# Kernel tuning notes

Hardware: AMD Instinct MI355X
Metric: run time of the kernel (lower is better)

The kernel has to match this reference:

```python
import jax, jax.numpy as jnp
import numpy as np

P, M, DG, F, H, DH = 2000, 150, 2000, 256, 4, 64
N1, N2 = P + M, P + DG          # adj1 nodes (patient+med), adj2 nodes (patient+diag)
E1, E2, EGP, EGM = 137600, 256000, 64000, 4800
GNN_LAYERS = 2
SA_HID = 128


def setup_inputs() -> dict:
    key = jax.random.key(0)
    ks = jax.random.split(key, 32)
    ri = lambda k, n, hi: jax.random.randint(k, (n,), 0, hi, dtype=jnp.int32)
    rn = lambda k, shape, scale: (jax.random.normal(k, shape, dtype=jnp.float32) * scale)
    inp = {
        'adj1_rows': ri(ks[0], E1, N1), 'adj1_cols': ri(ks[1], E1, N1),
        'adj1_vals': jax.random.uniform(ks[2], (E1,), dtype=jnp.float32),
        'adj2_rows': ri(ks[3], E2, N2), 'adj2_cols': ri(ks[4], E2, N2),
        'adj2_vals': jax.random.uniform(ks[5], (E2,), dtype=jnp.float32),
        'g0_src': ri(ks[6], EGP, P), 'g0_dst': ri(ks[7], EGP, P),
        'g1_src': ri(ks[8], EGP, P), 'g1_dst': ri(ks[9], EGP, P),
        'g2_src': ri(ks[10], EGM, M), 'g2_dst': ri(ks[11], EGM, M),
        'g3_src': ri(ks[12], EGM, M), 'g3_dst': ri(ks[13], EGM, M),
        'keepRate': 1,
        # learned parameters (xavier-ish scales)
        'pEmbed': rn(ks[14], (P, F), 0.05),
        'mEmbed': rn(ks[15], (M, F), 0.05),
        'dEmbed': rn(ks[16], (DG, F), 0.05),
        'gat_W': rn(ks[17], (4, F, H * DH), (2.0 / (F + H * DH)) ** 0.5),
        'gat_al': rn(ks[18], (4, H, DH), 0.1),
        'gat_ar': rn(ks[19], (4, H, DH), 0.1),
        'gat_b': jnp.zeros((4, H * DH), dtype=jnp.float32),
        'sa_W1': rn(ks[20], (H * DH, SA_HID), (2.0 / (H * DH + SA_HID)) ** 0.5),
        'sa_b1': jnp.zeros((SA_HID,), dtype=jnp.float32),
        'sa_W2': rn(ks[21], (SA_HID, 1), 0.1),
        'out_W': rn(ks[22], (2 * F, M), (2.0 / (2 * F + M)) ** 0.5),
        'out_b': jnp.zeros((M,), dtype=jnp.float32),
    }
    return inp


def _spmm(rows, cols, vals, x, n):
    # sparse adj @ x via gather + segment_sum
    return jax.ops.segment_sum(vals[:, None] * x[cols], rows, num_segments=n)


def _seg_softmax(e, seg, n):
    m = jax.ops.segment_max(e, seg, num_segments=n)          # [n, H]
    ex = jnp.exp(e - m[seg])
    s = jax.ops.segment_sum(ex, seg, num_segments=n)
    return ex / (s[seg] + 1e-9)


def _gat(h, W, al, ar, b, src, dst, n):
    # DGL GATConv, feat/attn dropout = 0, negative_slope = 0.2, activation = elu
    feat = (h @ W).reshape(n, H, DH)                          # [n, H, DH]
    el = (feat * al[None]).sum(-1)                            # [n, H]
    er = (feat * ar[None]).sum(-1)
    e = jax.nn.leaky_relu(el[src] + er[dst], negative_slope=0.2)  # [E, H]
    alpha = _seg_softmax(e, dst, n)                           # softmax over in-edges per dst
    out = jax.ops.segment_sum(alpha[:, :, None] * feat[src], dst, num_segments=n)
    out = out + b.reshape(1, H, DH)
    return jax.nn.elu(out).reshape(n, H * DH)


def _sem_att(z, W1, b1, W2):
    # z: [N, K, F]; shared projection; beta over K meta-paths
    w = (jnp.tanh(z @ W1 + b1) @ W2).mean(0)                  # [K, 1]
    beta = jax.nn.softmax(w, axis=0)                          # [K, 1]
    return (beta[None] * z).sum(1)                            # [N, F]


def reference(adj1_rows, adj1_cols, adj1_vals, adj2_rows, adj2_cols, adj2_vals,
              g0_src, g0_dst, g1_src, g1_dst, g2_src, g2_dst, g3_src, g3_dst,
              keepRate, pEmbed, mEmbed, dEmbed, gat_W, gat_al, gat_ar, gat_b,
              sa_W1, sa_b1, sa_W2, out_W, out_b):
    embeds1 = jnp.concatenate([pEmbed, mEmbed], axis=0)       # [N1, F]
    embeds2 = jnp.concatenate([pEmbed, dEmbed], axis=0)       # [N2, F]
    lat1, lat2 = embeds1, embeds2
    acc1 = jnp.zeros_like(embeds1)
    acc2 = jnp.zeros_like(embeds2)
    for _ in range(GNN_LAYERS):
        lat1 = jax.nn.leaky_relu(_spmm(adj1_rows, adj1_cols, adj1_vals, lat1, N1), negative_slope=0.5)
        lat2 = jax.nn.leaky_relu(_spmm(adj2_rows, adj2_cols, adj2_vals, lat2, N2), negative_slope=0.5)
        acc1 = acc1 + lat1
        acc2 = acc2 + lat2
    p1, m_gcn = acc1[:P], acc1[P:]
    p2, d_gcn = acc2[:P], acc2[P:]

    e0 = _gat(p1, gat_W[0], gat_al[0], gat_ar[0], gat_b[0], g0_src, g0_dst, P)
    e1 = _gat(p2, gat_W[1], gat_al[1], gat_ar[1], gat_b[1], g1_src, g1_dst, P)
    e2 = _gat(m_gcn, gat_W[2], gat_al[2], gat_ar[2], gat_b[2], g2_src, g2_dst, M)
    e3 = _gat(m_gcn, gat_W[3], gat_al[3], gat_ar[3], gat_b[3], g3_src, g3_dst, M)

    patient = _sem_att(jnp.stack([e0, e1], axis=1), sa_W1, sa_b1, sa_W2)  # [P, F]
    med = _sem_att(jnp.stack([e2, e3], axis=1), sa_W1, sa_b1, sa_W2)      # [M, F]

    # broadcasted pairwise concat -> ReLU -> Linear -> sum over pairing axis
    pm = jnp.concatenate([
        jnp.broadcast_to(patient[:, None, :], (P, M, F)),
        jnp.broadcast_to(med[None, :, :], (P, M, F)),
    ], axis=-1).reshape(P * M, 2 * F)
    simi = (jax.nn.relu(pm) @ out_W + out_b).reshape(P, M, M)
    simi_pm = simi.sum(axis=1)                                # [P, M]
    return (simi_pm, d_gcn, med, m_gcn, patient)
```

## Files before the change

### kernel.cpp

```cpp
#include <hip/hip_runtime.h>
#include <hip/hip_fp16.h>
#include <cmath>
#include <cstdint>

constexpr int P  = 2000, M = 150, DG = 2000, F = 256, H = 4, DH = 64;
constexpr int N1 = P + M;
constexpr int N2 = P + DG;
constexpr int E1 = 137600, E2 = 256000, EGP = 64000, EGM = 4800;
constexpr int SA_HID = 128;

constexpr int HO1 = E1, HO2 = E1 + E2, HO3 = HO2 + EGP, HO4 = HO3 + EGP,
              HO5 = HO4 + EGM, HOE = HO5 + EGM;

constexpr int CAP_A = 160;
constexpr int CAP_G = 96;
constexpr int OVF_CAP = 4096;

constexpr int CPAD = 16;

__device__ __forceinline__ float4 h4_to_f4(const __half* p) {
  union { ushort4 u4; __half2 h2[2]; } u;
  u.u4 = *(const ushort4*)p;
  float2 lo = __half22float2(u.h2[0]);
  float2 hi = __half22float2(u.h2[1]);
  return make_float4(lo.x, lo.y, hi.x, hi.y);
}
__device__ __forceinline__ void f4_to_h4(__half* p, float4 v) {
  union { ushort4 u4; __half2 h2[2]; } u;
  u.h2[0] = __float22half2_rn(make_float2(v.x, v.y));
  u.h2[1] = __float22half2_rn(make_float2(v.z, v.w));
  *(ushort4*)p = u.u4;
}

constexpr int CAST_CH = (P * F + M * F + DG * F) / 8;

__global__ __launch_bounds__(256) void k_build(
    const int* __restrict__ a1r, const int* __restrict__ a1c, const float* __restrict__ a1v,
    const int* __restrict__ a2r, const int* __restrict__ a2c, const float* __restrict__ a2v,
    const int* __restrict__ d0, const int* __restrict__ s0,
    const int* __restrict__ d1, const int* __restrict__ s1,
    const int* __restrict__ d2, const int* __restrict__ s2,
    const int* __restrict__ d3, const int* __restrict__ s3,
    int* cur1, uint2* ell1, int* cur2, uint2* ell2,
    int* cu0, unsigned* eg0, int* cu1, unsigned* eg1,
    int* cu2, unsigned* eg2, int* cu3, unsigned* eg3,
    int* __restrict__ ovf_n, int4* __restrict__ ovf,
    const float* __restrict__ pEf, const float* __restrict__ mEf,
    const float* __restrict__ dEf,
    __half* __restrict__ pEh, __half* __restrict__ mEh, __half* __restrict__ dEh) {
  int tid = blockIdx.x * 256 + threadIdx.x;
  int T = gridDim.x * 256;
  int seg[4], row[4]; unsigned p0[4], p1[4];
#pragma unroll
  for (int u = 0; u < 4; ++u) {
    int i = tid + u * T;
    seg[u] = -1;
    if (i < HOE) {
      if (i < HO1)      { seg[u] = 0; row[u] = a1r[i]; p0[u] = (unsigned)a1c[i]; p1[u] = __float_as_uint(a1v[i]); }
      else if (i < HO2) { int j = i - HO1; seg[u] = 1; row[u] = a2r[j]; p0[u] = (unsigned)a2c[j]; p1[u] = __float_as_uint(a2v[j]); }
      else if (i < HO3) { int j = i - HO2; seg[u] = 2; row[u] = d0[j]; p0[u] = (unsigned)s0[j]; }
      else if (i < HO4) { int j = i - HO3; seg[u] = 3; row[u] = d1[j]; p0[u] = (unsigned)s1[j]; }
      else if (i < HO5) { int j = i - HO4; seg[u] = 4; row[u] = d2[j]; p0[u] = (unsigned)s2[j]; }
      else              { int j = i - HO5; seg[u] = 5; row[u] = d3[j]; p0[u] = (unsigned)s3[j]; }
    }
  }
#pragma unroll
  for (int u = 0; u < 4; ++u) {
    int r = row[u];
    switch (seg[u]) {
      case 0: { int slot = atomicAdd(&cur1[(size_t)r * CPAD], 1);
        if (slot < CAP_A) ell1[(size_t)r * CAP_A + slot] = make_uint2(p0[u], p1[u]);
        else { int o = atomicAdd(&ovf_n[0], 1); if (o < OVF_CAP) ovf[0 * OVF_CAP + o] = make_int4(r, (int)p0[u], (int)p1[u], 0); } } break;
      case 1: { int slot = atomicAdd(&cur2[(size_t)r * CPAD], 1);
        if (slot < CAP_A) ell2[(size_t)r * CAP_A + slot] = make_uint2(p0[u], p1[u]);
        else { int o = atomicAdd(&ovf_n[1], 1); if (o < OVF_CAP) ovf[1 * OVF_CAP + o] = make_int4(r, (int)p0[u], (int)p1[u], 0); } } break;
      case 2: { int slot = atomicAdd(&cu0[(size_t)r * CPAD], 1);
        if (slot < CAP_G) eg0[(size_t)r * CAP_G + slot] = p0[u];
        else { int o = atomicAdd(&ovf_n[2], 1); if (o < OVF_CAP) ovf[2 * OVF_CAP + o] = make_int4(r, (int)p0[u], 0, 0); } } break;
      case 3: { int slot = atomicAdd(&cu1[(size_t)r * CPAD], 1);
        if (slot < CAP_G) eg1[(size_t)r * CAP_G + slot] = p0[u];
        else { int o = atomicAdd(&ovf_n[3], 1); if (o < OVF_CAP) ovf[3 * OVF_CAP + o] = make_int4(r, (int)p0[u], 0, 0); } } break;
      case 4: { int slot = atomicAdd(&cu2[(size_t)r * CPAD], 1);
        if (slot < CAP_G) eg2[(size_t)r * CAP_G + slot] = p0[u];
        else { int o = atomicAdd(&ovf_n[4], 1); if (o < OVF_CAP) ovf[4 * OVF_CAP + o] = make_int4(r, (int)p0[u], 0, 0); } } break;
      case 5: { int slot = atomicAdd(&cu3[(size_t)r * CPAD], 1);
        if (slot < CAP_G) eg3[(size_t)r * CAP_G + slot] = p0[u];
        else { int o = atomicAdd(&ovf_n[5], 1); if (o < OVF_CAP) ovf[5 * OVF_CAP + o] = make_int4(r, (int)p0[u], 0, 0); } } break;
      default: break;
    }
  }
  for (int c = tid; c < CAST_CH; c += T) {
    int j = c * 8;
    const float* src; __half* dst;
    if (j < P * F)              { src = pEf + j;               dst = pEh + j; }
    else if (j < P * F + M * F) { src = mEf + (j - P * F);     dst = mEh + (j - P * F); }
    else                        { src = dEf + (j - P*F - M*F); dst = dEh + (j - P*F - M*F); }
    float4 a = *(const float4*)src, b = *(const float4*)(src + 4);
    f4_to_h4(dst, a);
    f4_to_h4(dst + 4, b);
  }
}

template<int LAYER>
__global__ __launch_bounds__(256) void k_spmm(
    const int* __restrict__ cur1, const uint2* __restrict__ ell1,
    const int* __restrict__ cur2, const uint2* __restrict__ ell2,
    const int* __restrict__ ovf_n, const int4* __restrict__ ovf,
    const __half* __restrict__ pEh, const __half* __restrict__ mEh,
    const __half* __restrict__ dEh,
    float* __restrict__ lat1f, float* __restrict__ lat2f,
    __half* __restrict__ lat1h, __half* __restrict__ lat2h,
    float* __restrict__ acc1, float* __restrict__ acc2,
    float* __restrict__ out_mgcn, float* __restrict__ out_dgcn) {
  int grp = (blockIdx.x * 256 + threadIdx.x) >> 7;
  int lane = threadIdx.x & 63;
  int wh   = (threadIdx.x >> 6) & 1;
  int gl   = threadIdx.x >> 7;
  bool g2 = grp >= N1;
  int row = g2 ? grp - N1 : grp;
  const uint2* pe = (g2 ? ell2 : ell1) + (size_t)row * CAP_A;
  const __half* latinh = g2 ? lat2h : lat1h;
  const __half* tailEh = g2 ? dEh : mEh;
  int deg = (g2 ? cur2 : cur1)[(size_t)row * CPAD];
  int dn = deg < CAP_A ? deg : CAP_A;
  int fo = lane << 2;
  float4 s = {0.f, 0.f, 0.f, 0.f};
  auto fetch = [&](int c) -> float4 {
    const __half* b;
    if (LAYER == 1) b = (c < P) ? (pEh + (size_t)c * F) : (tailEh + (size_t)(c - P) * F);
    else            b = latinh + (size_t)c * F;
    return h4_to_f4(b + fo);
  };
  int i = wh;
  for (; i + 15 <= dn; i += 16) {
    uint2 m[8]; float4 a[8];
#pragma unroll
    for (int u = 0; u < 8; ++u) m[u] = pe[i + 2 * u];
#pragma unroll
    for (int u = 0; u < 8; ++u) a[u] = fetch((int)m[u].x);
#pragma unroll
    for (int u = 0; u < 8; ++u) {
      float v = __uint_as_float(m[u].y);
      s.x += v * a[u].x; s.y += v * a[u].y; s.z += v * a[u].z; s.w += v * a[u].w;
    }
  }
  for (; i < dn; i += 2) {
    uint2 m = pe[i];
    float v = __uint_as_float(m.y);
    float4 a = fetch((int)m.x);
    s.x += v * a.x; s.y += v * a.y; s.z += v * a.z; s.w += v * a.w;
  }
  __shared__ float part[2][F];
  if (wh == 1) *(float4*)&part[gl][fo] = s;
  __syncthreads();
  if (wh == 1) return;
  {
    float4 p = *(const float4*)&part[gl][fo];
    s.x += p.x; s.y += p.y; s.z += p.z; s.w += p.w;
  }
  {
    int gi = g2 ? 1 : 0;
    int on = ovf_n[gi];
    if (on > 0) {
      const int4* ol = ovf + gi * OVF_CAP;
      for (int k = 0; k < on; ++k) {
        int4 e = ol[k];
        if (e.x == row) {
          float v = __int_as_float(e.z);
          float4 a = fetch(e.y);
          s.x += v * a.x; s.y += v * a.y; s.z += v * a.z; s.w += v * a.w;
        }
      }
    }
  }
  float4 l;
  l.x = s.x > 0.f ? s.x : 0.5f * s.x;
  l.y = s.y > 0.f ? s.y : 0.5f * s.y;
  l.z = s.z > 0.f ? s.z : 0.5f * s.z;
  l.w = s.w > 0.f ? s.w : 0.5f * s.w;
  if (LAYER == 1) {
    *(float4*)((g2 ? lat2f : lat1f) + (size_t)row * F + fo) = l;
    f4_to_h4((g2 ? lat2h : lat1h) + (size_t)row * F + fo, l);
  } else {
    const float* latf = g2 ? lat2f : lat1f;
    float4 b = *(const float4*)(latf + (size_t)row * F + fo);
    float4 a = {b.x + l.x, b.y + l.y, b.z + l.z, b.w + l.w};
    *(float4*)((g2 ? acc2 : acc1) + (size_t)row * F + fo) = a;
    if (row >= P)
      *(float4*)((g2 ? out_dgcn : out_mgcn) + (size_t)(row - P) * F + fo) = a;
  }
}

constexpr int FR  = 8;
constexpr int NB0 = (P + FR - 1) / FR;
constexpr int NB2 = (M + FR - 1) / FR;
constexpr int FEAT_BLOCKS = 2 * NB0 + 2 * NB2;

__global__ __launch_bounds__(256) void k_gat_feat_all(
    const float* __restrict__ acc1, const float* __restrict__ acc2,
    const float* __restrict__ gat_W, const float* __restrict__ gat_al,
    const float* __restrict__ gat_ar,
    __half* __restrict__ f0, __half* __restrict__ f1,
    __half* __restrict__ f2, __half* __restrict__ f3,
    float* __restrict__ el, float* __restrict__ er) {
  int b = blockIdx.x;
  int g, rb, n; const float* h; __half* fout;
  if (b < NB0)            { g = 0; rb = b;              n = P; h = acc1; fout = f0; }
  else if (b < 2 * NB0)   { g = 1; rb = b - NB0;        n = P; h = acc2; fout = f1; }
  else if (b < 2*NB0+NB2) { g = 2; rb = b - 2 * NB0;    n = M; h = acc1 + (size_t)P * F; fout = f2; }
  else                    { g = 3; rb = b - 2*NB0 - NB2; n = M; h = acc1 + (size_t)P * F; fout = f3; }
  int elo = (g == 0) ? 0 : (g == 1) ? P * H : (g == 2) ? 2 * P * H : (2 * P + M) * H;
  const float* W = gat_W + (size_t)g * F * F;
  __shared__ float hs[FR][F];
  int t = threadIdx.x;
  int r0 = rb * FR;
  for (int q = t; q < FR * 64; q += 256) {
    int r = q >> 6, ln = q & 63;
    int row = r0 + r;
    float4 v = {0.f, 0.f, 0.f, 0.f};
    if (row < n) v = *(const float4*)(h + (size_t)row * F + (ln << 2));
    *(float4*)&hs[r][ln << 2] = v;
  }
  __syncthreads();
  float acc[FR];
#pragma unroll
  for (int r = 0; r < FR; ++r) acc[r] = 0.f;
  for (int k = 0; k < F; k += 4) {
    float w0 = W[(size_t)k * F + t],       w1 = W[(size_t)(k + 1) * F + t],
          w2 = W[(size_t)(k + 2) * F + t], w3 = W[(size_t)(k + 3) * F + t];
#pragma unroll
    for (int r = 0; r < FR; ++r) {
      float4 h4 = *(const float4*)&hs[r][k];
      acc[r] += h4.x * w0 + h4.y * w1 + h4.z * w2 + h4.w * w3;
    }
  }
  int head = t >> 6, d = t & 63;
  float av = gat_al[g * H * DH + head * DH + d];
  float rv = gat_ar[g * H * DH + head * DH + d];
#pragma unroll
  for (int r = 0; r < FR; ++r) {
    int row = r0 + r;
    if (row < n) {
      fout[(size_t)row * F + t] = __float2half_rn(acc[r]);
      float cl = acc[r] * av, cr = acc[r] * rv;
      for (int o = 32; o > 0; o >>= 1) {
        cl += __shfl_down(cl, o, 64);
        cr += __shfl_down(cr, o, 64);
      }
      if (d == 0) { el[elo + row * H + head] = cl; er[elo + row * H + head] = cr; }
    }
  }
}

__global__ __launch_bounds__(256) void k_gat_agg_all(
    const int* __restrict__ cu0, const unsigned* __restrict__ eg0,
    const int* __restrict__ cu1, const unsigned* __restrict__ eg1,
    const int* __restrict__ cu2, const unsigned* __restrict__ eg2,
    const int* __restrict__ cu3, const unsigned* __restrict__ eg3,
    const int* __restrict__ ovf_n, const int4* __restrict__ ovf,
    const float* __restrict__ el, const float* __restrict__ er,
    const __half* __restrict__ f0, const __half* __restrict__ f1,
    const __half* __restrict__ f2, const __half* __restrict__ f3,
    const float* __restrict__ gat_b,
    float* __restrict__ e0, float* __restrict__ e1,
    float* __restrict__ e2, float* __restrict__ e3) {
  int grp = (blockIdx.x * 256 + threadIdx.x) >> 7;
  int lane = threadIdx.x & 63;
  int wh   = (threadIdx.x >> 6) & 1;
  int gl   = threadIdx.x >> 7;
  int g, row; const int* cu; const unsigned* eg; const __half* feat; float* out; int elo;
  if (grp < P)            { g = 0; row = grp;             cu = cu0; eg = eg0; feat = f0; out = e0; elo = 0; }
  else if (grp < 2 * P)   { g = 1; row = grp - P;         cu = cu1; eg = eg1; feat = f1; out = e1; elo = P * H; }
  else if (grp < 2*P + M) { g = 2; row = grp - 2 * P;     cu = cu2; eg = eg2; feat = f2; out = e2; elo = 2 * P * H; }
  else                    { g = 3; row = grp - 2 * P - M; cu = cu3; eg = eg3; feat = f3; out = e3; elo = (2 * P + M) * H; }
  int head = lane >> 4;
  int fo = lane << 2;
  const float* elb = el + elo;
  float erv = er[elo + row * H + head];
  int deg = cu[(size_t)row * CPAD];
  int dn = deg < CAP_G ? deg : CAP_G;
  const unsigned* ps = eg + (size_t)row * CAP_G;
  int on = ovf_n[2 + g];
  const int4* ol = ovf + (2 + g) * OVF_CAP;
  float mx = -3.4e38f;
  int i = wh;
  for (; i + 7 <= dn; i += 8) {
    int s0 = (int)ps[i], s1 = (int)ps[i + 2], s2 = (int)ps[i + 4], s3 = (int)ps[i + 6];
    float a = elb[s0 * H + head] + erv, b = elb[s1 * H + head] + erv,
          c = elb[s2 * H + head] + erv, d = elb[s3 * H + head] + erv;
    a = a > 0.f ? a : 0.2f * a; b = b > 0.f ? b : 0.2f * b;
    c = c > 0.f ? c : 0.2f * c; d = d > 0.f ? d : 0.2f * d;
    mx = fmaxf(mx, fmaxf(fmaxf(a, b), fmaxf(c, d)));
  }
  for (; i < dn; i += 2) {
    float a = elb[(int)ps[i] * H + head] + erv;
    a = a > 0.f ? a : 0.2f * a;
    mx = fmaxf(mx, a);
  }
  if (wh == 0 && on > 0) {
    for (int k = 0; k < on; ++k) {
      int4 e = ol[k];
      if (e.x == row) {
        float a = elb[e.y * H + head] + erv;
        a = a > 0.f ? a : 0.2f * a;
        mx = fmaxf(mx, a);
      }
    }
  }
  __shared__ float mxs[2][2][64];
  mxs[gl][wh][lane] = mx;
  __syncthreads();
  mx = fmaxf(mxs[gl][0][lane], mxs[gl][1][lane]);
  float ssum = 0.f;
  float4 acc = {0.f, 0.f, 0.f, 0.f};
  i = wh;
  for (; i + 7 <= dn; i += 8) {
    int s0 = (int)ps[i], s1 = (int)ps[i + 2], s2 = (int)ps[i + 4], s3 = (int)ps[i + 6];
    float a = elb[s0 * H + head] + erv; a = a > 0.f ? a : 0.2f * a;
    float b = elb[s1 * H + head] + erv; b = b > 0.f ? b : 0.2f * b;
    float c = elb[s2 * H + head] + erv; c = c > 0.f ? c : 0.2f * c;
    float d = elb[s3 * H + head] + erv; d = d > 0.f ? d : 0.2f * d;
    float x0 = expf(a - mx), x1 = expf(b - mx), x2 = expf(c - mx), x3 = expf(d - mx);
    float4 q0 = h4_to_f4(feat + (size_t)s0 * F + fo);
    float4 q1 = h4_to_f4(feat + (size_t)s1 * F + fo);
    float4 q2 = h4_to_f4(feat + (size_t)s2 * F + fo);
    float4 q3 = h4_to_f4(feat + (size_t)s3 * F + fo);
    ssum += (x0 + x1) + (x2 + x3);
    acc.x += x0 * q0.x + x1 * q1.x + x2 * q2.x + x3 * q3.x;
    acc.y += x0 * q0.y + x1 * q1.y + x2 * q2.y + x3 * q3.y;
    acc.z += x0 * q0.z + x1 * q1.z + x2 * q2.z + x3 * q3.z;
    acc.w += x0 * q0.w + x1 * q1.w + x2 * q2.w + x3 * q3.w;
  }
  for (; i + 3 <= dn; i += 4) {
    int s0 = (int)ps[i], s1 = (int)ps[i + 2];
    float a = elb[s0 * H + head] + erv; a = a > 0.f ? a : 0.2f * a;
    float b = elb[s1 * H + head] + erv; b = b > 0.f ? b : 0.2f * b;
    float x0 = expf(a - mx), x1 = expf(b - mx);
    float4 q0 = h4_to_f4(feat + (size_t)s0 * F + fo);
    float4 q1 = h4_to_f4(feat + (size_t)s1 * F + fo);
    ssum += x0 + x1;
    acc.x += x0 * q0.x + x1 * q1.x;
    acc.y += x0 * q0.y + x1 * q1.y;
    acc.z += x0 * q0.z + x1 * q1.z;
    acc.w += x0 * q0.w + x1 * q1.w;
  }
  for (; i < dn; i += 2) {
    int s0 = (int)ps[i];
    float a = elb[s0 * H + head] + erv; a = a > 0.f ? a : 0.2f * a;
    float x0 = expf(a - mx);
    float4 q0 = h4_to_f4(feat + (size_t)s0 * F + fo);
    ssum += x0;
    acc.x += x0 * q0.x; acc.y += x0 * q0.y; acc.z += x0 * q0.z; acc.w += x0 * q0.w;
  }
  __shared__ float4 pacc[2][64];
  __shared__ float  pss[2][64];
  if (wh == 1) { pacc[gl][lane] = acc; pss[gl][lane] = ssum; }
  __syncthreads();
  if (wh == 1) return;
  {
    float4 pa = pacc[gl][lane];
    acc.x += pa.x; acc.y += pa.y; acc.z += pa.z; acc.w += pa.w;
    ssum += pss[gl][lane];
  }
  if (on > 0) {
    for (int k = 0; k < on; ++k) {
      int4 e = ol[k];
      if (e.x == row) {
        float a = elb[e.y * H + head] + erv; a = a > 0.f ? a : 0.2f * a;
        float x0 = expf(a - mx);
        float4 q0 = h4_to_f4(feat + (size_t)e.y * F + fo);
        ssum += x0;
        acc.x += x0 * q0.x; acc.y += x0 * q0.y; acc.z += x0 * q0.z; acc.w += x0 * q0.w;
      }
    }
  }
  float inv = 1.f / (ssum + 1e-9f);
  const float* bb = gat_b + g * F + fo;
  float4 v = {acc.x * inv + bb[0], acc.y * inv + bb[1],
              acc.z * inv + bb[2], acc.w * inv + bb[3]};
  v.x = v.x > 0.f ? v.x : expm1f(v.x);
  v.y = v.y > 0.f ? v.y : expm1f(v.y);
  v.z = v.z > 0.f ? v.z : expm1f(v.z);
  v.w = v.w > 0.f ? v.w : expm1f(v.w);
  *(float4*)(out + (size_t)row * F + fo) = v;
}

constexpr int SR  = 4;
constexpr int SB0 = (P + SR - 1) / SR;
constexpr int SB2 = (M + SR - 1) / SR;
constexpr int SEM_BLOCKS = 2 * SB0 + 2 * SB2;

__global__ __launch_bounds__(128) void k_sem_w_all(
    const float* __restrict__ e0, const float* __restrict__ e1,
    const float* __restrict__ e2, const float* __restrict__ e3,
    const float* __restrict__ W1, const float* __restrict__ b1,
    const float* __restrict__ W2, float* __restrict__ w) {
  int b = blockIdx.x;
  int zid, rb, n; const float* z;
  if (b < SB0)            { zid = 0; rb = b;             n = P; z = e0; }
  else if (b < 2 * SB0)   { zid = 1; rb = b - SB0;       n = P; z = e1; }
  else if (b < 2*SB0+SB2) { zid = 2; rb = b - 2 * SB0;   n = M; z = e2; }
  else                    { zid = 3; rb = b - 2*SB0-SB2; n = M; z = e3; }
  __shared__ float zs[SR][F];
  int t = threadIdx.x;
  int r0 = rb * SR;
  for (int q = t; q < SR * 64; q += 128) {
    int r = q >> 6, ln = q & 63;
    int row = r0 + r;
    float4 v = {0.f, 0.f, 0.f, 0.f};
    if (row < n) v = *(const float4*)(z + (size_t)row * F + (ln << 2));
    *(float4*)&zs[r][ln << 2] = v;
  }
  __syncthreads();
  float hid[SR];
#pragma unroll
  for (int r = 0; r < SR; ++r) hid[r] = b1[t];
  for (int k = 0; k < F; k += 4) {
    float w0 = W1[(size_t)k * SA_HID + t],       w1 = W1[(size_t)(k + 1) * SA_HID + t],
          w2 = W1[(size_t)(k + 2) * SA_HID + t], w3 = W1[(size_t)(k + 3) * SA_HID + t];
#pragma unroll
    for (int r = 0; r < SR; ++r) {
      float4 z4 = *(const float4*)&zs[r][k];
      hid[r] += z4.x * w0 + z4.y * w1 + z4.z * w2 + z4.w * w3;
    }
  }
  float w2v = W2[t];
  float local = 0.f;
  for (int r = 0; r < SR; ++r) {
    int row = r0 + r;
    if (row < n) local += tanhf(hid[r]) * w2v;
  }
  for (int o = 32; o > 0; o >>= 1) local += __shfl_down(local, o, 64);
  __shared__ float pp[2];
  if ((t & 63) == 0) pp[t >> 6] = local;
  __syncthreads();
  if (t == 0) atomicAdd(&w[zid], pp[0] + pp[1]);
}

constexpr int FIN_R = 4;
__global__ __launch_bounds__(256) void k_final_all(
    const float* __restrict__ e0, const float* __restrict__ e1,
    const float* __restrict__ e2, const float* __restrict__ e3,
    const float* __restrict__ w, const float* __restrict__ outW,
    const float* __restrict__ outb,
    float* __restrict__ out_med, float* __restrict__ out_pat,
    float* __restrict__ simi) {
  int t = threadIdx.x;
  float mm0 = w[2] * (1.f / M), mm1 = w[3] * (1.f / M);
  float mmx = fmaxf(mm0, mm1);
  float bm0 = expf(mm0 - mmx), bm1 = expf(mm1 - mmx);
  float msc = 1.f / (bm0 + bm1);
  bm0 *= msc; bm1 *= msc;
  float pm0 = w[0] * (1.f / P), pm1 = w[1] * (1.f / P);
  float pmx = fmaxf(pm0, pm1);
  float bp0 = expf(pm0 - pmx), bp1 = expf(pm1 - pmx);
  float psc = 1.f / (bp0 + bp1);
  bp0 *= psc; bp1 *= psc;
  int r0 = blockIdx.x * FIN_R;
  int pr = t >> 6, pln = t & 63;
  size_t poff = (size_t)(r0 + pr) * F + (pln << 2);
  float4 pu0 = *(const float4*)(e0 + poff);
  float4 pu1 = *(const float4*)(e1 + poff);
  constexpr int MED4 = M * F / 4;
  float4 rs = {0.f, 0.f, 0.f, 0.f};
  bool wr_med = (blockIdx.x == 0);
  for (int j = t; j < MED4; j += 512) {
    float4 u0 = ((const float4*)e2)[j], u1 = ((const float4*)e3)[j];
    float4 v0, v1;
    bool second = (j + 256) < MED4;
    if (second) { v0 = ((const float4*)e2)[j + 256]; v1 = ((const float4*)e3)[j + 256]; }
    float4 r = {bm0 * u0.x + bm1 * u1.x, bm0 * u0.y + bm1 * u1.y,
                bm0 * u0.z + bm1 * u1.z, bm0 * u0.w + bm1 * u1.w};
    if (wr_med) ((float4*)out_med)[j] = r;
    rs.x += r.x > 0.f ? r.x : 0.f;
    rs.y += r.y > 0.f ? r.y : 0.f;
    rs.z += r.z > 0.f ? r.z : 0.f;
    rs.w += r.w > 0.f ? r.w : 0.f;
    if (second) {
      float4 r2 = {bm0 * v0.x + bm1 * v1.x, bm0 * v0.y + bm1 * v1.y,
                   bm0 * v0.z + bm1 * v1.z, bm0 * v0.w + bm1 * v1.w};
      if (wr_med) ((float4*)out_med)[j + 256] = r2;
      rs.x += r2.x > 0.f ? r2.x : 0.f;
      rs.y += r2.y > 0.f ? r2.y : 0.f;
      rs.z += r2.z > 0.f ? r2.z : 0.f;
      rs.w += r2.w > 0.f ? r2.w : 0.f;
    }
  }
  __shared__ float psh[FIN_R][F];
  {
    float4 v = {bp0 * pu0.x + bp1 * pu1.x, bp0 * pu0.y + bp1 * pu1.y,
                bp0 * pu0.z + bp1 * pu1.z, bp0 * pu0.w + bp1 * pu1.w};
    *(float4*)(out_pat + poff) = v;
    v.x = v.x > 0.f ? v.x : 0.f; v.y = v.y > 0.f ? v.y : 0.f;
    v.z = v.z > 0.f ? v.z : 0.f; v.w = v.w > 0.f ? v.w : 0.f;
    *(float4*)&psh[pr][pln << 2] = v;
  }
  __shared__ float4 sv4[4][64];
  sv4[t >> 6][t & 63] = rs;
  __syncthreads();
  __shared__ float sv[F];
  if (t < 64) {
    float4 a = sv4[0][t], b = sv4[1][t], c = sv4[2][t], d = sv4[3][t];
    sv[t * 4 + 0] = a.x + b.x + c.x + d.x;
    sv[t * 4 + 1] = a.y + b.y + c.y + d.y;
    sv[t * 4 + 2] = a.z + b.z + c.z + d.z;
    sv[t * 4 + 3] = a.w + b.w + c.w + d.w;
  }
  __syncthreads();
  if (t < M) {
    float acc[FIN_R];
#pragma unroll
    for (int r = 0; r < FIN_R; ++r) acc[r] = 0.f;
    float cv = (float)M * outb[t];
    for (int f = 0; f < F; f += 4) {
      float w0 = outW[(size_t)f * M + t],       w1 = outW[(size_t)(f + 1) * M + t],
            w2 = outW[(size_t)(f + 2) * M + t], w3 = outW[(size_t)(f + 3) * M + t];
      float b0 = outW[(size_t)(F + f) * M + t],     b1 = outW[(size_t)(F + f + 1) * M + t],
            b2 = outW[(size_t)(F + f + 2) * M + t], b3 = outW[(size_t)(F + f + 3) * M + t];
      cv += sv[f] * b0 + sv[f + 1] * b1 + sv[f + 2] * b2 + sv[f + 3] * b3;
#pragma unroll
      for (int r = 0; r < FIN_R; ++r) {
        float4 p4 = *(const float4*)&psh[r][f];
        acc[r] += p4.x * w0 + p4.y * w1 + p4.z * w2 + p4.w * w3;
      }
    }
#pragma unroll
    for (int r = 0; r < FIN_R; ++r)
      simi[(size_t)(r0 + r) * M + t] = (float)M * acc[r] + cv;
  }
}

extern "C" void kernel_launch(void* const* d_in, const int* in_sizes, int n_in,
                              void* d_out, int out_size, void* d_ws, size_t ws_size,
                              hipStream_t stream) {
  const int*   adj1_rows = (const int*)d_in[0];
  const int*   adj1_cols = (const int*)d_in[1];
  const float* adj1_vals = (const float*)d_in[2];
  const int*   adj2_rows = (const int*)d_in[3];
  const int*   adj2_cols = (const int*)d_in[4];
  const float* adj2_vals = (const float*)d_in[5];
  const int*   g0_src = (const int*)d_in[6];
  const int*   g0_dst = (const int*)d_in[7];
  const int*   g1_src = (const int*)d_in[8];
  const int*   g1_dst = (const int*)d_in[9];
  const int*   g2_src = (const int*)d_in[10];
  const int*   g2_dst = (const int*)d_in[11];
  const int*   g3_src = (const int*)d_in[12];
  const int*   g3_dst = (const int*)d_in[13];
  const float* pE     = (const float*)d_in[15];
  const float* mE     = (const float*)d_in[16];
  const float* dE     = (const float*)d_in[17];
  const float* gat_W  = (const float*)d_in[18];
  const float* gat_al = (const float*)d_in[19];
  const float* gat_ar = (const float*)d_in[20];
  const float* gat_b  = (const float*)d_in[21];
  const float* sa_W1  = (const float*)d_in[22];
  const float* sa_b1  = (const float*)d_in[23];
  const float* sa_W2  = (const float*)d_in[24];
  const float* out_W  = (const float*)d_in[25];
  const float* out_b  = (const float*)d_in[26];

  int* ip = (int*)d_ws;
  int* cur1 = ip; ip += (size_t)N1 * CPAD;
  int* cur2 = ip; ip += (size_t)N2 * CPAD;
  int* cu0  = ip; ip += (size_t)P * CPAD;
  int* cu1  = ip; ip += (size_t)P * CPAD;
  int* cu2  = ip; ip += (size_t)M * CPAD;
  int* cu3  = ip; ip += (size_t)M * CPAD;
  int* ovf_n = ip; ip += 6;
  float* wbuf = (float*)ip; ip += 4;
  size_t memset_bytes = (size_t)((char*)ip - (char*)d_ws);

  uintptr_t up = ((uintptr_t)ip + 15) & ~(uintptr_t)15;
  int4* ovf = (int4*)up;
  uint2* ell1 = (uint2*)(ovf + 6 * OVF_CAP);
  uint2* ell2 = ell1 + (size_t)N1 * CAP_A;
  unsigned* eg0 = (unsigned*)(ell2 + (size_t)N2 * CAP_A);
  unsigned* eg1 = eg0 + (size_t)P * CAP_G;
  unsigned* eg2 = eg1 + (size_t)P * CAP_G;
  unsigned* eg3 = eg2 + (size_t)M * CAP_G;
  __half* hp = (__half*)(eg3 + (size_t)M * CAP_G);
  __half* pEh   = hp; hp += (size_t)P * F;
  __half* mEh   = hp; hp += (size_t)M * F;
  __half* dEh   = hp; hp += (size_t)DG * F;
  __half* lat1h = hp; hp += (size_t)N1 * F;
  __half* lat2h = hp; hp += (size_t)N2 * F;
  __half* f0h   = hp; hp += (size_t)P * F;
  __half* f1h   = hp; hp += (size_t)P * F;
  __half* f2h   = hp; hp += (size_t)M * F;
  __half* f3h   = hp; hp += (size_t)M * F;
  float* fp = (float*)hp;
  float* lat1f = fp; fp += (size_t)N1 * F;
  float* lat2f = fp; fp += (size_t)N2 * F;
  float* acc1  = fp; fp += (size_t)N1 * F;
  float* acc2  = fp; fp += (size_t)N2 * F;
  float* el    = fp; fp += (size_t)(2 * P + 2 * M) * H;
  float* er    = fp; fp += (size_t)(2 * P + 2 * M) * H;
  float* e0b   = fp; fp += (size_t)P * F;
  float* e1b   = fp; fp += (size_t)P * F;
  float* e2b   = fp; fp += (size_t)M * F;
  float* e3b   = fp; fp += (size_t)M * F;

  float* out_simi = (float*)d_out;
  float* out_dgcn = out_simi + (size_t)P * M;
  float* out_med  = out_dgcn + (size_t)DG * F;
  float* out_mgcn = out_med  + (size_t)M * F;
  float* out_pat  = out_mgcn + (size_t)M * F;

  hipMemsetAsync(d_ws, 0, memset_bytes, stream);

  int eb = ((HOE + 3) / 4 + 255) / 256;
  k_build<<<eb, 256, 0, stream>>>(adj1_rows, adj1_cols, adj1_vals,
                                  adj2_rows, adj2_cols, adj2_vals,
                                  g0_dst, g0_src, g1_dst, g1_src,
                                  g2_dst, g2_src, g3_dst, g3_src,
                                  cur1, ell1, cur2, ell2,
                                  cu0, eg0, cu1, eg1, cu2, eg2, cu3, eg3,
                                  ovf_n, ovf,
                                  pE, mE, dE, pEh, mEh, dEh);

  int sb = (N1 + N2) / 2;
  k_spmm<1><<<sb, 256, 0, stream>>>(cur1, ell1, cur2, ell2, ovf_n, ovf,
                                    pEh, mEh, dEh, lat1f, lat2f, lat1h, lat2h,
                                    acc1, acc2, out_mgcn, out_dgcn);
  k_spmm<2><<<sb, 256, 0, stream>>>(cur1, ell1, cur2, ell2, ovf_n, ovf,
                                    pEh, mEh, dEh, lat1f, lat2f, lat1h, lat2h,
                                    acc1, acc2, out_mgcn, out_dgcn);

  k_gat_feat_all<<<FEAT_BLOCKS, 256, 0, stream>>>(acc1, acc2, gat_W, gat_al, gat_ar,
                                                  f0h, f1h, f2h, f3h, el, er);
  int ab = (2 * P + 2 * M) / 2;
  k_gat_agg_all<<<ab, 256, 0, stream>>>(cu0, eg0, cu1, eg1, cu2, eg2, cu3, eg3,
                                        ovf_n, ovf, el, er, f0h, f1h, f2h, f3h, gat_b,
                                        e0b, e1b, e2b, e3b);

  k_sem_w_all<<<SEM_BLOCKS, 128, 0, stream>>>(e0b, e1b, e2b, e3b, sa_W1, sa_b1, sa_W2, wbuf);

  k_final_all<<<P / FIN_R, 256, 0, stream>>>(e0b, e1b, e2b, e3b, wbuf, out_W, out_b,
                                             out_med, out_pat, out_simi);
}
```

Before: 304.6 us.

## Use 16-byte gathers in SpMM and single-pass online softmax in GAT aggregation

The SpMM kernel now has each half-wavefront handle a different neighbor, loading 8 halves (16 bytes) per lane. The two halves are combined with a cross-lane shuffle, which halves the number of load instructions per edge. The GAT aggregation kernel replaces its separate max pass with an online softmax that rescales the running sum and accumulator, then merges the two wavefront partials with max-aware scaling. This removes a second traversal over the edge list and the el gathers, at the cost of extra exp calls and multiplies per step.

New measurement: 340.1 us. 11.6% more time.

```diff
diff --git a/kernel.cpp b/kernel.cpp
--- a/kernel.cpp
+++ b/kernel.cpp
@@ -30,6 +30,16 @@
   u.h2[0] = __float22half2_rn(make_float2(v.x, v.y));
   u.h2[1] = __float22half2_rn(make_float2(v.z, v.w));
   *(ushort4*)p = u.u4;
+}
+__device__ __forceinline__ void h8_to_f8(const __half* p, float4& lo, float4& hi) {
+  union { uint4 u; __half2 h2[4]; } uu;
+  uu.u = *(const uint4*)p;
+  float2 a0 = __half22float2(uu.h2[0]);
+  float2 a1 = __half22float2(uu.h2[1]);
+  float2 a2 = __half22float2(uu.h2[2]);
+  float2 a3 = __half22float2(uu.h2[3]);
+  lo = make_float4(a0.x, a0.y, a1.x, a1.y);
+  hi = make_float4(a2.x, a2.y, a3.x, a3.y);
 }
 
 constexpr int CAST_CH = (P * F + M * F + DG * F) / 8;
@@ -116,6 +126,9 @@
   int lane = threadIdx.x & 63;
   int wh   = (threadIdx.x >> 6) & 1;
   int gl   = threadIdx.x >> 7;
+  int half = lane >> 5;
+  int hl   = lane & 31;
+  int fo8  = hl << 3;
   bool g2 = grp >= N1;
   int row = g2 ? grp - N1 : grp;
   const uint2* pe = (g2 ? ell2 : ell1) + (size_t)row * CAP_A;
@@ -123,40 +136,65 @@
   const __half* tailEh = g2 ? dEh : mEh;
   int deg = (g2 ? cur2 : cur1)[(size_t)row * CPAD];
   int dn = deg < CAP_A ? deg : CAP_A;
-  int fo = lane << 2;
-  float4 s = {0.f, 0.f, 0.f, 0.f};
-  auto fetch = [&](int c) -> float4 {
-    const __half* b;
-    if (LAYER == 1) b = (c < P) ? (pEh + (size_t)c * F) : (tailEh + (size_t)(c - P) * F);
-    else            b = latinh + (size_t)c * F;
-    return h4_to_f4(b + fo);
+  float4 sA = {0.f, 0.f, 0.f, 0.f}, sB = {0.f, 0.f, 0.f, 0.f};
+  auto base = [&](int c) -> const __half* {
+    if (LAYER == 1) return (c < P) ? (pEh + (size_t)c * F) : (tailEh + (size_t)(c - P) * F);
+    return latinh + (size_t)c * F;
+  };
+  auto fetch8 = [&](int c, float4& lo, float4& hi) {
+    h8_to_f8(base(c) + fo8, lo, hi);
   };
   int i = wh;
   for (; i + 15 <= dn; i += 16) {
-    uint2 m[8]; float4 a[8];
+    uint2 m[8];
 #pragma unroll
     for (int u = 0; u < 8; ++u) m[u] = pe[i + 2 * u];
-#pragma unroll
-    for (int u = 0; u < 8; ++u) a[u] = fetch((int)m[u].x);
-#pragma unroll
-    for (int u = 0; u < 8; ++u) {
-      float v = __uint_as_float(m[u].y);
-      s.x += v * a[u].x; s.y += v * a[u].y; s.z += v * a[u].z; s.w += v * a[u].w;
-    }
-  }
-  for (; i < dn; i += 2) {
-    uint2 m = pe[i];
-    float v = __uint_as_float(m.y);
-    float4 a = fetch((int)m.x);
-    s.x += v * a.x; s.y += v * a.y; s.z += v * a.z; s.w += v * a.w;
-  }
+    float4 lo[4], hi[4];
+#pragma unroll
+    for (int u = 0; u < 4; ++u) {
+      uint2 me = half ? m[2 * u + 1] : m[2 * u];
+      fetch8((int)me.x, lo[u], hi[u]);
+    }
+#pragma unroll
+    for (int u = 0; u < 4; ++u) {
+      uint2 me = half ? m[2 * u + 1] : m[2 * u];
+      float v = __uint_as_float(me.y);
+      sA.x += v * lo[u].x; sA.y += v * lo[u].y; sA.z += v * lo[u].z; sA.w += v * lo[u].w;
+      sB.x += v * hi[u].x; sB.y += v * hi[u].y; sB.z += v * hi[u].z; sB.w += v * hi[u].w;
+    }
+  }
+  for (; i + 3 <= dn; i += 4) {
+    uint2 m0 = pe[i], m1 = pe[i + 2];
+    uint2 me = half ? m1 : m0;
+    float4 lo, hi; fetch8((int)me.x, lo, hi);
+    float v = __uint_as_float(me.y);
+    sA.x += v * lo.x; sA.y += v * lo.y; sA.z += v * lo.z; sA.w += v * lo.w;
+    sB.x += v * hi.x; sB.y += v * hi.y; sB.z += v * hi.z; sB.w += v * hi.w;
+  }
+  if (i < dn) {
+    uint2 m0 = pe[i];
+    uint2 me = half ? make_uint2(0u, 0u) : m0;
+    float4 lo, hi; fetch8((int)me.x, lo, hi);
+    float v = __uint_as_float(me.y);
+    sA.x += v * lo.x; sA.y += v * lo.y; sA.z += v * lo.z; sA.w += v * lo.w;
+    sB.x += v * hi.x; sB.y += v * hi.y; sB.z += v * hi.z; sB.w += v * hi.w;
+  }
+  sA.x += __shfl_down(sA.x, 32, 64); sA.y += __shfl_down(sA.y, 32, 64);
+  sA.z += __shfl_down(sA.z, 32, 64); sA.w += __shfl_down(sA.w, 32, 64);
+  sB.x += __shfl_down(sB.x, 32, 64); sB.y += __shfl_down(sB.y, 32, 64);
+  sB.z += __shfl_down(sB.z, 32, 64); sB.w += __shfl_down(sB.w, 32, 64);
   __shared__ float part[2][F];
-  if (wh == 1) *(float4*)&part[gl][fo] = s;
+  if (wh == 1 && half == 0) {
+    *(float4*)&part[gl][fo8]     = sA;
+    *(float4*)&part[gl][fo8 + 4] = sB;
+  }
   __syncthreads();
   if (wh == 1) return;
-  {
-    float4 p = *(const float4*)&part[gl][fo];
-    s.x += p.x; s.y += p.y; s.z += p.z; s.w += p.w;
+  if (half == 0) {
+    float4 pa = *(const float4*)&part[gl][fo8];
+    float4 pb = *(const float4*)&part[gl][fo8 + 4];
+    sA.x += pa.x; sA.y += pa.y; sA.z += pa.z; sA.w += pa.w;
+    sB.x += pb.x; sB.y += pb.y; sB.z += pb.z; sB.w += pb.w;
   }
   {
     int gi = g2 ? 1 : 0;
@@ -167,27 +205,46 @@
         int4 e = ol[k];
         if (e.x == row) {
           float v = __int_as_float(e.z);
-          float4 a = fetch(e.y);
-          s.x += v * a.x; s.y += v * a.y; s.z += v * a.z; s.w += v * a.w;
+          float4 lo, hi; fetch8(e.y, lo, hi);
+          sA.x += v * lo.x; sA.y += v * lo.y; sA.z += v * lo.z; sA.w += v * lo.w;
+          sB.x += v * hi.x; sB.y += v * hi.y; sB.z += v * hi.z; sB.w += v * hi.w;
         }
       }
     }
   }
-  float4 l;
-  l.x = s.x > 0.f ? s.x : 0.5f * s.x;
-  l.y = s.y > 0.f ? s.y : 0.5f * s.y;
-  l.z = s.z > 0.f ? s.z : 0.5f * s.z;
-  l.w = s.w > 0.f ? s.w : 0.5f * s.w;
+  if (half != 0) return;
+  float4 lA, lB;
+  lA.x = sA.x > 0.f ? sA.x : 0.5f * sA.x;
+  lA.y = sA.y > 0.f ? sA.y : 0.5f * sA.y;
+  lA.z = sA.z > 0.f ? sA.z : 0.5f * sA.z;
+  lA.w = sA.w > 0.f ? sA.w : 0.5f * sA.w;
+  lB.x = sB.x > 0.f ? sB.x : 0.5f * sB.x;
+  lB.y = sB.y > 0.f ? sB.y : 0.5f * sB.y;
+  lB.z = sB.z > 0.f ? sB.z : 0.5f * sB.z;
+  lB.w = sB.w > 0.f ? sB.w : 0.5f * sB.w;
+  size_t off = (size_t)row * F + fo8;
   if (LAYER == 1) {
-    *(float4*)((g2 ? lat2f : lat1f) + (size_t)row * F + fo) = l;
-    f4_to_h4((g2 ? lat2h : lat1h) + (size_t)row * F + fo, l);
+    float* lf = (g2 ? lat2f : lat1f);
+    *(float4*)(lf + off) = lA;
+    *(float4*)(lf + off + 4) = lB;
+    __half* lh = (g2 ? lat2h : lat1h);
+    f4_to_h4(lh + off, lA);
+    f4_to_h4(lh + off + 4, lB);
   } else {
     const float* latf = g2 ? lat2f : lat1f;
-    float4 b = *(const float4*)(latf + (size_t)row * F + fo);
-    float4 a = {b.x + l.x, b.y + l.y, b.z + l.z, b.w + l.w};
-    *(float4*)((g2 ? acc2 : acc1) + (size_t)row * F + fo) = a;
-    if (row >= P)
-      *(float4*)((g2 ? out_dgcn : out_mgcn) + (size_t)(row - P) * F + fo) = a;
+    float4 b0 = *(const float4*)(latf + off);
+    float4 b1 = *(const float4*)(latf + off + 4);
+    float4 a0 = {b0.x + lA.x, b0.y + lA.y, b0.z + lA.z, b0.w + lA.w};
+    float4 a1 = {b1.x + lB.x, b1.y + lB.y, b1.z + lB.z, b1.w + lB.w};
+    float* ac = (g2 ? acc2 : acc1);
+    *(float4*)(ac + off) = a0;
+    *(float4*)(ac + off + 4) = a1;
+    if (row >= P) {
+      float* og = (g2 ? out_dgcn : out_mgcn);
+      size_t ooff = (size_t)(row - P) * F + fo8;
+      *(float4*)(og + ooff) = a0;
+      *(float4*)(og + ooff + 4) = a1;
+    }
   }
 }
 
@@ -282,95 +339,92 @@
   const unsigned* ps = eg + (size_t)row * CAP_G;
   int on = ovf_n[2 + g];
   const int4* ol = ovf + (2 + g) * OVF_CAP;
-  float mx = -3.4e38f;
+  float m = -3.4e38f, ssum = 0.f;
+  float4 acc = {0.f, 0.f, 0.f, 0.f};
   int i = wh;
-  for (; i + 7 <= dn; i += 8) {
-    int s0 = (int)ps[i], s1 = (int)ps[i + 2], s2 = (int)ps[i + 4], s3 = (int)ps[i + 6];
-    float a = elb[s0 * H + head] + erv, b = elb[s1 * H + head] + erv,
-          c = elb[s2 * H + head] + erv, d = elb[s3 * H + head] + erv;
-    a = a > 0.f ? a : 0.2f * a; b = b > 0.f ? b : 0.2f * b;
-    c = c > 0.f ? c : 0.2f * c; d = d > 0.f ? d : 0.2f * d;
-    mx = fmaxf(mx, fmaxf(fmaxf(a, b), fmaxf(c, d)));
-  }
-  for (; i < dn; i += 2) {
-    float a = elb[(int)ps[i] * H + head] + erv;
-    a = a > 0.f ? a : 0.2f * a;
-    mx = fmaxf(mx, a);
-  }
-  if (wh == 0 && on > 0) {
-    for (int k = 0; k < on; ++k) {
-      int4 e = ol[k];
-      if (e.x == row) {
-        float a = elb[e.y * H + head] + erv;
-        a = a > 0.f ? a : 0.2f * a;
-        mx = fmaxf(mx, a);
-      }
-    }
-  }
-  __shared__ float mxs[2][2][64];
-  mxs[gl][wh][lane] = mx;
-  __syncthreads();
-  mx = fmaxf(mxs[gl][0][lane], mxs[gl][1][lane]);
-  float ssum = 0.f;
-  float4 acc = {0.f, 0.f, 0.f, 0.f};
-  i = wh;
   for (; i + 7 <= dn; i += 8) {
     int s0 = (int)ps[i], s1 = (int)ps[i + 2], s2 = (int)ps[i + 4], s3 = (int)ps[i + 6];
     float a = elb[s0 * H + head] + erv; a = a > 0.f ? a : 0.2f * a;
     float b = elb[s1 * H + head] + erv; b = b > 0.f ? b : 0.2f * b;
     float c = elb[s2 * H + head] + erv; c = c > 0.f ? c : 0.2f * c;
     float d = elb[s3 * H + head] + erv; d = d > 0.f ? d : 0.2f * d;
-    float x0 = expf(a - mx), x1 = expf(b - mx), x2 = expf(c - mx), x3 = expf(d - mx);
+    float nm = fmaxf(m, fmaxf(fmaxf(a, b), fmaxf(c, d)));
+    float sc = expf(m - nm);
+    float x0 = expf(a - nm), x1 = expf(b - nm), x2 = expf(c - nm), x3 = expf(d - nm);
     float4 q0 = h4_to_f4(feat + (size_t)s0 * F + fo);
     float4 q1 = h4_to_f4(feat + (size_t)s1 * F + fo);
     float4 q2 = h4_to_f4(feat + (size_t)s2 * F + fo);
     float4 q3 = h4_to_f4(feat + (size_t)s3 * F + fo);
-    ssum += (x0 + x1) + (x2 + x3);
-    acc.x += x0 * q0.x + x1 * q1.x + x2 * q2.x + x3 * q3.x;
-    acc.y += x0 * q0.y + x1 * q1.y + x2 * q2.y + x3 * q3.y;
-    acc.z += x0 * q0.z + x1 * q1.z + x2 * q2.z + x3 * q3.z;
-    acc.w += x0 * q0.w + x1 * q1.w + x2 * q2.w + x3 * q3.w;
+    ssum = ssum * sc + (x0 + x1) + (x2 + x3);
+    acc.x = acc.x * sc + x0 * q0.x + x1 * q1.x + x2 * q2.x + x3 * q3.x;
+    acc.y = acc.y * sc + x0 * q0.y + x1 * q1.y + x2 * q2.y + x3 * q3.y;
+    acc.z = acc.z * sc + x0 * q0.z + x1 * q1.z + x2 * q2.z + x3 * q3.z;
+    acc.w = acc.w * sc + x0 * q0.w + x1 * q1.w + x2 * q2.w + x3 * q3.w;
+    m = nm;
   }
   for (; i + 3 <= dn; i += 4) {
     int s0 = (int)ps[i], s1 = (int)ps[i + 2];
     float a = elb[s0 * H + head] + erv; a = a > 0.f ? a : 0.2f * a;
     float b = elb[s1 * H + head] + erv; b = b > 0.f ? b : 0.2f * b;
-    float x0 = expf(a - mx), x1 = expf(b - mx);
+    float nm = fmaxf(m, fmaxf(a, b));
+    float sc = expf(m - nm);
+    float x0 = expf(a - nm), x1 = expf(b - nm);
     float4 q0 = h4_to_f4(feat + (size_t)s0 * F + fo);
     float4 q1 = h4_to_f4(feat + (size_t)s1 * F + fo);
-    ssum += x0 + x1;
-    acc.x += x0 * q0.x + x1 * q1.x;
-    acc.y += x0 * q0.y + x1 * q1.y;
-    acc.z += x0 * q0.z + x1 * q1.z;
-    acc.w += x0 * q0.w + x1 * q1.w;
+    ssum = ssum * sc + x0 + x1;
+    acc.x = acc.x * sc + x0 * q0.x + x1 * q1.x;
+    acc.y = acc.y * sc + x0 * q0.y + x1 * q1.y;
+    acc.z = acc.z * sc + x0 * q0.z + x1 * q1.z;
+    acc.w = acc.w * sc + x0 * q0.w + x1 * q1.w;
+    m = nm;
   }
   for (; i < dn; i += 2) {
     int s0 = (int)ps[i];
     float a = elb[s0 * H + head] + erv; a = a > 0.f ? a : 0.2f * a;
-    float x0 = expf(a - mx);
+    float nm = fmaxf(m, a);
+    float sc = expf(m - nm);
+    float x0 = expf(a - nm);
     float4 q0 = h4_to_f4(feat + (size_t)s0 * F + fo);
-    ssum += x0;
-    acc.x += x0 * q0.x; acc.y += x0 * q0.y; acc.z += x0 * q0.z; acc.w += x0 * q0.w;
-  }
+    ssum = ssum * sc + x0;
+    acc.x = acc.x * sc + x0 * q0.x;
+    acc.y = acc.y * sc + x0 * q0.y;
+    acc.z = acc.z * sc + x0 * q0.z;
+    acc.w = acc.w * sc + x0 * q0.w;
+    m = nm;
+  }
+  __shared__ float  pm[2][64];
+  __shared__ float  pss[2][64];
   __shared__ float4 pacc[2][64];
-  __shared__ float  pss[2][64];
-  if (wh == 1) { pacc[gl][lane] = acc; pss[gl][lane] = ssum; }
+  if (wh == 1) { pm[gl][lane] = m; pss[gl][lane] = ssum; pacc[gl][lane] = acc; }
   __syncthreads();
   if (wh == 1) return;
   {
-    float4 pa = pacc[gl][lane];
-    acc.x += pa.x; acc.y += pa.y; acc.z += pa.z; acc.w += pa.w;
-    ssum += pss[gl][lane];
+    float m1 = pm[gl][lane], s1 = pss[gl][lane];
+    float4 a1 = pacc[gl][lane];
+    float nm = fmaxf(m, m1);
+    float c0 = expf(m - nm), c1 = expf(m1 - nm);
+    ssum = ssum * c0 + s1 * c1;
+    acc.x = acc.x * c0 + a1.x * c1;
+    acc.y = acc.y * c0 + a1.y * c1;
+    acc.z = acc.z * c0 + a1.z * c1;
+    acc.w = acc.w * c0 + a1.w * c1;
+    m = nm;
   }
   if (on > 0) {
     for (int k = 0; k < on; ++k) {
       int4 e = ol[k];
       if (e.x == row) {
         float a = elb[e.y * H + head] + erv; a = a > 0.f ? a : 0.2f * a;
-        float x0 = expf(a - mx);
+        float nm = fmaxf(m, a);
+        float sc = expf(m - nm);
+        float x0 = expf(a - nm);
         float4 q0 = h4_to_f4(feat + (size_t)e.y * F + fo);
-        ssum += x0;
-        acc.x += x0 * q0.x; acc.y += x0 * q0.y; acc.z += x0 * q0.z; acc.w += x0 * q0.w;
+        ssum = ssum * sc + x0;
+        acc.x = acc.x * sc + x0 * q0.x;
+        acc.y = acc.y * sc + x0 * q0.y;
+        acc.z = acc.z * sc + x0 * q0.z;
+        acc.w = acc.w * sc + x0 * q0.w;
+        m = nm;
       }
     }
   }
```
